# Performance work log

Hardware: AMD Instinct MI355X
Metric: run time of the kernel (lower is better)

## Reference

```python
import jax, jax.numpy as jnp
import numpy as np

B, S, D = 4, 2048, 1024
N_HEAD, D_HEAD = 16, 64


def setup_inputs() -> dict:
    key = jax.random.key(0)
    ks = jax.random.split(key, 9)
    sd = 0.02
    x = jax.random.normal(ks[0], (B, S, D), dtype=jnp.float32)
    # causal mask: True = masked (future positions)
    causal = jnp.triu(jnp.ones((S, S), dtype=bool), k=1)
    attn_mask = jnp.broadcast_to(causal, (B, S, S))
    Wq = jax.random.normal(ks[1], (D, N_HEAD * D_HEAD), dtype=jnp.float32) * sd
    bq = jnp.zeros((N_HEAD * D_HEAD,), dtype=jnp.float32)
    Wk = jax.random.normal(ks[2], (D, N_HEAD * D_HEAD), dtype=jnp.float32) * sd
    bk = jnp.zeros((N_HEAD * D_HEAD,), dtype=jnp.float32)
    Wv = jax.random.normal(ks[3], (D, N_HEAD * D_HEAD), dtype=jnp.float32) * sd
    bv = jnp.zeros((N_HEAD * D_HEAD,), dtype=jnp.float32)
    Wo = jax.random.normal(ks[4], (N_HEAD * D_HEAD, D), dtype=jnp.float32) * sd
    bo = jnp.zeros((D,), dtype=jnp.float32)
    return {"x": x, "attn_mask": attn_mask, "Wq": Wq, "bq": bq,
            "Wk": Wk, "bk": bk, "Wv": Wv, "bv": bv, "Wo": Wo, "bo": bo}


def reference(x, attn_mask, Wq, bq, Wk, bk, Wv, bv, Wo, bo):
    b, s, _ = x.shape
    scale = 1.0 / (D_HEAD ** 0.5)
    # QKV projections -> [b, n_head, s, d_head]
    def split_heads(y):
        return y.reshape(b, s, N_HEAD, D_HEAD).transpose(0, 2, 1, 3)
    q = split_heads(x @ Wq + bq)
    k = split_heads(x @ Wk + bk)
    v = split_heads(x @ Wv + bv)
    scores = jnp.einsum('bhqd,bhkd->bhqk', q, k) * scale
    scores = jnp.where(attn_mask[:, None, :, :], jnp.float32(-1e9), scores)
    attn_prob = jax.nn.softmax(scores, axis=-1)
    context = jnp.einsum('bhqk,bhkd->bhqd', attn_prob, v)
    context = context.transpose(0, 2, 1, 3).reshape(b, s, N_HEAD * D_HEAD)
    output = context @ Wo + bo
    return (output, attn_prob)
```

## Files before the change

kernel.cpp:

```cpp
#include <hip/hip_runtime.h>
#include <hip/hip_bf16.h>

typedef unsigned short u16;
typedef __attribute__((ext_vector_type(8))) short bf16x8;
typedef __attribute__((ext_vector_type(4))) float f32x4;

#define S_LEN  2048
#define DMODEL 1024
#define NHEAD  16
#define DH     64
#define BATCH  4
#define QBLK   128
#define KBLK   64
#define SWZ(row, c) (((c) ^ ((row) & 7)))

__device__ inline u16 f2bf(float f) {
  union { float f; unsigned u; } v; v.f = f;
  unsigned u = v.u;
  return (u16)((u + 0x7FFFu + ((u >> 16) & 1u)) >> 16);
}

__device__ inline f32x4 mfma16(bf16x8 a, bf16x8 b, f32x4 c) {
  return __builtin_amdgcn_mfma_f32_16x16x32_bf16(a, b, c, 0, 0, 0);
}

__device__ inline void gload_lds16(const u16* g, u16* l) {
  __builtin_amdgcn_global_load_lds(
      (const __attribute__((address_space(1))) void*)g,
      (__attribute__((address_space(3))) void*)l, 16, 0, 0);
}

__global__ __launch_bounds__(256) void k_convert_x(const float* __restrict__ x,
                                                   u16* __restrict__ xb) {
  int idx = blockIdx.x * 256 + threadIdx.x;
  const float4* p = (const float4*)(x + (size_t)idx * 8);
  float4 a = p[0], b = p[1];
  bf16x8 o;
  o[0] = (short)f2bf(a.x); o[1] = (short)f2bf(a.y);
  o[2] = (short)f2bf(a.z); o[3] = (short)f2bf(a.w);
  o[4] = (short)f2bf(b.x); o[5] = (short)f2bf(b.y);
  o[6] = (short)f2bf(b.z); o[7] = (short)f2bf(b.w);
  *(bf16x8*)(xb + (size_t)idx * 8) = o;
}

__global__ __launch_bounds__(256) void k_wT4(const float* __restrict__ W0,
                                             const float* __restrict__ W1,
                                             const float* __restrict__ W2,
                                             const float* __restrict__ W3,
                                             u16* __restrict__ WtBase) {
  __shared__ float T[32][33];
  int z = blockIdx.z;
  const float* W = (z == 0) ? W0 : (z == 1) ? W1 : (z == 2) ? W2 : W3;
  u16* Wt = WtBase + (size_t)z * DMODEL * DMODEL;
  int tx = threadIdx.x, ty = threadIdx.y;
  int n0 = blockIdx.x * 32, k0 = blockIdx.y * 32;
  for (int i = 0; i < 4; ++i)
    T[ty + i * 8][tx] = W[(size_t)(k0 + ty + i * 8) * DMODEL + n0 + tx];
  __syncthreads();
  for (int i = 0; i < 4; ++i)
    Wt[(size_t)(n0 + ty + i * 8) * DMODEL + k0 + tx] = f2bf(T[tx][ty + i * 8]);
}

__global__ __launch_bounds__(256) void k_gemm_qkv(const u16* __restrict__ A,
                                                  const u16* __restrict__ Wcat,
                                                  const float* __restrict__ bq,
                                                  const float* __restrict__ bk,
                                                  const float* __restrict__ bv,
                                                  u16* __restrict__ Qh,
                                                  u16* __restrict__ Kh,
                                                  u16* __restrict__ Vc) {
  const int K = 1024;
  __shared__ u16 As[128 * 32];
  __shared__ u16 Bs[128 * 32];
  int tid = threadIdx.x, w = tid >> 6, l = tid & 63;
  int f = blockIdx.x;
  int xcd = f & 7, i = f >> 3;
  int sb = i >> 6;
  int t = i & 63;
  int bm = xcd * 8 + (t & 7);
  int bn = sb * 8 + (t >> 3);
  int wr = w >> 1, wc = w & 1;
  f32x4 acc[4][4];
  for (int ii = 0; ii < 4; ++ii)
    for (int j = 0; j < 4; ++j) acc[ii][j] = (f32x4){0.f, 0.f, 0.f, 0.f};
  const u16* Ablk = A + (size_t)bm * 128 * K;
  const u16* Bblk = Wcat + (size_t)bn * 128 * K;

  for (int ks = 0; ks < K / 32; ++ks) {
    int k0 = ks * 32;
    __syncthreads();
    for (int r = 0; r < 2; ++r) {
      int c = r * 256 + tid;
      int row = c >> 2, c4 = c & 3;
      gload_lds16(Ablk + (size_t)row * K + k0 + c4 * 8, &As[c * 8]);
      gload_lds16(Bblk + (size_t)row * K + k0 + c4 * 8, &Bs[c * 8]);
    }
    __syncthreads();
    bf16x8 af[4], bfr[4];
    for (int mt = 0; mt < 4; ++mt)
      af[mt] = *(const bf16x8*)&As[(wr * 64 + mt * 16 + (l & 15)) * 32 + (l >> 4) * 8];
    for (int nt = 0; nt < 4; ++nt)
      bfr[nt] = *(const bf16x8*)&Bs[(wc * 64 + nt * 16 + (l & 15)) * 32 + (l >> 4) * 8];
    for (int mt = 0; mt < 4; ++mt)
      for (int nt = 0; nt < 4; ++nt)
        acc[mt][nt] = mfma16(af[mt], bfr[nt], acc[mt][nt]);
  }

  int region = (bn * 128) >> 10;
  const float* bias = (region == 0) ? bq : (region == 1) ? bk : bv;
  u16* dst = (region == 0) ? Qh : (region == 1) ? Kh : Vc;

  for (int mt = 0; mt < 4; ++mt)
    for (int nt = 0; nt < 4; ++nt) {
      int colg = bn * 128 + wc * 64 + nt * 16 + (l & 15);
      int col = colg & 1023;
      float bsv = bias[col];
      for (int r = 0; r < 4; ++r) {
        int row = bm * 128 + wr * 64 + mt * 16 + (l >> 4) * 4 + r;
        float v = acc[mt][nt][r] + bsv;
        if (region == 2) {
          dst[(size_t)row * 1024 + col] = f2bf(v);
        } else {
          int b = row >> 11, s = row & 2047, h = col >> 6, d = col & 63;
          dst[(((size_t)(b * NHEAD + h)) * S_LEN + s) * DH + d] = f2bf(v);
        }
      }
    }
}

__global__ __launch_bounds__(256) void k_gemm_out(const u16* __restrict__ A,
                                                  const u16* __restrict__ Bt,
                                                  const float* __restrict__ bias,
                                                  float* __restrict__ Cout) {
  const int K = 1024, N = 1024;
  __shared__ u16 As[128 * 32];
  __shared__ u16 Bs[128 * 32];
  int tid = threadIdx.x, w = tid >> 6, l = tid & 63;
  int f = blockIdx.x;
  int xcd = f & 7, i = f >> 3;
  int bm = xcd * 8 + (i & 7);
  int bn = i >> 3;
  int wr = w >> 1, wc = w & 1;
  f32x4 acc[4][4];
  for (int ii = 0; ii < 4; ++ii)
    for (int j = 0; j < 4; ++j) acc[ii][j] = (f32x4){0.f, 0.f, 0.f, 0.f};
  const u16* Ablk = A + (size_t)bm * 128 * K;
  const u16* Bblk = Bt + (size_t)bn * 128 * K;

  for (int ks = 0; ks < K / 32; ++ks) {
    int k0 = ks * 32;
    __syncthreads();
    for (int r = 0; r < 2; ++r) {
      int c = r * 256 + tid;
      int row = c >> 2, c4 = c & 3;
      gload_lds16(Ablk + (size_t)row * K + k0 + c4 * 8, &As[c * 8]);
      gload_lds16(Bblk + (size_t)row * K + k0 + c4 * 8, &Bs[c * 8]);
    }
    __syncthreads();
    bf16x8 af[4], bfr[4];
    for (int mt = 0; mt < 4; ++mt)
      af[mt] = *(const bf16x8*)&As[(wr * 64 + mt * 16 + (l & 15)) * 32 + (l >> 4) * 8];
    for (int nt = 0; nt < 4; ++nt)
      bfr[nt] = *(const bf16x8*)&Bs[(wc * 64 + nt * 16 + (l & 15)) * 32 + (l >> 4) * 8];
    for (int mt = 0; mt < 4; ++mt)
      for (int nt = 0; nt < 4; ++nt)
        acc[mt][nt] = mfma16(af[mt], bfr[nt], acc[mt][nt]);
  }

  for (int mt = 0; mt < 4; ++mt)
    for (int nt = 0; nt < 4; ++nt) {
      int col = bn * 128 + wc * 64 + nt * 16 + (l & 15);
      float bsv = bias[col];
      for (int r = 0; r < 4; ++r) {
        int row = bm * 128 + wr * 64 + mt * 16 + (l >> 4) * 4 + r;
        Cout[(size_t)row * N + col] = acc[mt][nt][r] + bsv;
      }
    }
}

__global__ __launch_bounds__(256) void k_vT(const u16* __restrict__ Vc,
                                            u16* __restrict__ Vt) {
  __shared__ u16 T[64][65];
  int bh = blockIdx.x, st = blockIdx.y;
  int b = bh >> 4, h = bh & 15;
  int s0 = st * 64;
  int tid = threadIdx.x;
  int row = tid >> 2, seg = tid & 3;
  const u16* src = Vc + ((size_t)(b * S_LEN + s0 + row)) * DMODEL + h * DH + seg * 16;
  bf16x8 v0 = *(const bf16x8*)src;
  bf16x8 v1 = *(const bf16x8*)(src + 8);
  for (int i = 0; i < 8; ++i) T[row][seg * 16 + i] = (u16)v0[i];
  for (int i = 0; i < 8; ++i) T[row][seg * 16 + 8 + i] = (u16)v1[i];
  __syncthreads();
  int d = row, sc = seg * 16;
  bf16x8 o0, o1;
  for (int i = 0; i < 8; ++i) o0[i] = (short)T[sc + i][d];
  for (int i = 0; i < 8; ++i) o1[i] = (short)T[sc + 8 + i][d];
  u16* dst = Vt + ((size_t)bh * DH + d) * S_LEN + s0 + sc;
  *(bf16x8*)dst = o0;
  *(bf16x8*)(dst + 8) = o1;
}


#define LOADK(KF, J0)                                                          \
  for (int kk_ = 0; kk_ < 2; ++kk_)                                            \
    for (int nt_ = 0; nt_ < 4; ++nt_)                                          \
      KF[kk_][nt_] = *(const bf16x8*)(Kg + (size_t)((J0) + nt_ * 16 + ln) * DH \
                                      + kk_ * 32 + lg * 8);

#define P1TILE(KF, J0)                                                         \
  {                                                                            \
    const int j0_ = (J0);                                                      \
    f32x4 acc[2][4];                                                           \
    for (int mt = 0; mt < 2; ++mt)                                             \
      for (int nt = 0; nt < 4; ++nt) acc[mt][nt] = (f32x4){0.f, 0.f, 0.f, 0.f};\
    for (int kk = 0; kk < 2; ++kk)                                             \
      for (int mt = 0; mt < 2; ++mt)                                           \
        for (int nt = 0; nt < 4; ++nt)                                         \
          acc[mt][nt] = mfma16(qf[mt][kk], KF[kk][nt], acc[mt][nt]);           \
    bool mask_ = (j0_ >= q0);                                                  \
    for (int mt = 0; mt < 2; ++mt)                                             \
      for (int r = 0; r < 4; ++r) {                                            \
        int rl = w * 32 + mt * 16 + lg * 4 + r;                                \
        float x0 = acc[mt][0][r] * scale2;                                     \
        float x1 = acc[mt][1][r] * scale2;                                     \
        float x2 = acc[mt][2][r] * scale2;                                     \
        float x3 = acc[mt][3][r] * scale2;                                     \
        if (mask_) {                                                           \
          if (j0_ + 0 + ln > q0 + rl) x0 = -1e9f;                              \
          if (j0_ + 16 + ln > q0 + rl) x1 = -1e9f;                             \
          if (j0_ + 32 + ln > q0 + rl) x2 = -1e9f;                             \
          if (j0_ + 48 + ln > q0 + rl) x3 = -1e9f;                             \
        }                                                                      \
        float s = __builtin_amdgcn_exp2f(x0) + __builtin_amdgcn_exp2f(x1) +    \
                  __builtin_amdgcn_exp2f(x2) + __builtin_amdgcn_exp2f(x3);     \
        s += __shfl_xor(s, 1);                                                 \
        s += __shfl_xor(s, 2);                                                 \
        s += __shfl_xor(s, 4);                                                 \
        s += __shfl_xor(s, 8);                                                 \
        lrow[mt][r] += s;                                                      \
      }                                                                        \
  }

#define P2TILE(KFC, KFN, KB, PRE)                                              \
  {                                                                            \
    const int j0_ = (KB) * KBLK;                                               \
    bf16x8 vb_[2][4];                                                          \
    for (int kk = 0; kk < 2; ++kk)                                             \
      for (int nt = 0; nt < 4; ++nt)                                           \
        vb_[kk][nt] = *(const bf16x8*)(Vg + (size_t)(nt * 16 + ln) * S_LEN +   \
                                       j0_ + kk * 32 + lg * 8);                \
    f32x4 acc[2][4];                                                           \
    for (int mt = 0; mt < 2; ++mt)                                             \
      for (int nt = 0; nt < 4; ++nt) acc[mt][nt] = (f32x4){0.f, 0.f, 0.f, 0.f};\
    for (int kk = 0; kk < 2; ++kk)                                             \
      for (int mt = 0; mt < 2; ++mt)                                           \
        for (int nt = 0; nt < 4; ++nt)                                         \
          acc[mt][nt] = mfma16(qf[mt][kk], KFC[kk][nt], acc[mt][nt]);          \
    if (PRE) { LOADK(KFN, j0_ + KBLK); }                                       \
    bool mask_ = (j0_ >= q0);                                                  \
    for (int mt = 0; mt < 2; ++mt)                                             \
      for (int r = 0; r < 4; ++r) {                                            \
        int rl = w * 32 + mt * 16 + lg * 4 + r;                                \
        float il = ilrow[mt][r];                                               \
        float* prow = Pg + (size_t)(q0 + rl) * S_LEN + j0_;                    \
        for (int nt = 0; nt < 4; ++nt) {                                       \
          int cl = nt * 16 + ln;                                               \
          float v = acc[mt][nt][r] * scale2;                                   \
          if (mask_ && (j0_ + cl > q0 + rl)) v = -1e9f;                        \
          float p = __builtin_amdgcn_exp2f(v) * il;                            \
          __builtin_nontemporal_store(p, prow + cl);                           \
          Ps[rl * 64 + SWZ(rl, cl >> 3) * 8 + (cl & 7)] = f2bf(p);             \
        }                                                                      \
      }                                                                        \
    for (int kk = 0; kk < 2; ++kk) {                                           \
      bf16x8 pa[2];                                                            \
      for (int mt = 0; mt < 2; ++mt) {                                         \
        int row = w * 32 + mt * 16 + ln;                                       \
        pa[mt] = *(const bf16x8*)&Ps[row * 64 + SWZ(row, kk * 4 + lg) * 8];    \
      }                                                                        \
      for (int mt = 0; mt < 2; ++mt)                                           \
        for (int nt = 0; nt < 4; ++nt)                                         \
          octx[mt][nt] = mfma16(pa[mt], vb_[kk][nt], octx[mt][nt]);            \
    }                                                                          \
  }

__global__ __launch_bounds__(256) void k_attn(const u16* __restrict__ Qh,
                                              const u16* __restrict__ Kh,
                                              const u16* __restrict__ Vt,
                                              float* __restrict__ P,
                                              u16* __restrict__ ctx) {
  __shared__ u16 Ps[QBLK * KBLK];

  int flat = blockIdx.x;
  int xcd = flat & 7, idx = flat >> 3;
  int bh = xcd * 8 + (idx >> 4);
  int qb = 15 - (idx & 15);
  int q0 = qb * QBLK;
  int tid = threadIdx.x, w = tid >> 6, l = tid & 63;
  const int lg = l >> 4, ln = l & 15;
  const u16* Qg = Qh + (size_t)bh * S_LEN * DH;
  const u16* Kg = Kh + (size_t)bh * S_LEN * DH;
  const u16* Vg = Vt + (size_t)bh * DH * S_LEN;
  float* Pg = P + (size_t)bh * S_LEN * S_LEN;

  bf16x8 qf[2][2];
  for (int mt = 0; mt < 2; ++mt)
    for (int kk = 0; kk < 2; ++kk)
      qf[mt][kk] = *(const bf16x8*)(Qg + (size_t)(q0 + w * 32 + mt * 16 + ln) * DH +
                                    kk * 32 + lg * 8);

  const int nkb = q0 / KBLK + QBLK / KBLK;
  const float scale2 = 0.18033688011112042f;

  float lrow[2][4];
  for (int mt = 0; mt < 2; ++mt)
    for (int r = 0; r < 4; ++r) lrow[mt][r] = 0.f;

  {
    bf16x8 kfA[2][4], kfB[2][4];
    LOADK(kfA, 0);
    for (int kb = 0; kb < nkb; kb += 2) {
      LOADK(kfB, (kb + 1) * KBLK);
      P1TILE(kfA, kb * KBLK);
      if (kb + 2 < nkb) LOADK(kfA, (kb + 2) * KBLK);
      P1TILE(kfB, (kb + 1) * KBLK);
    }
  }
  float ilrow[2][4];
  for (int mt = 0; mt < 2; ++mt)
    for (int r = 0; r < 4; ++r) ilrow[mt][r] = 1.f / lrow[mt][r];

  f32x4 octx[2][4];
  for (int mt = 0; mt < 2; ++mt)
    for (int nt = 0; nt < 4; ++nt) octx[mt][nt] = (f32x4){0.f, 0.f, 0.f, 0.f};

  {
    bf16x8 kfA[2][4], kfB[2][4];
    LOADK(kfA, 0);
    for (int kb = 0; kb < nkb; kb += 2) {
      P2TILE(kfA, kfB, kb, 1);
      P2TILE(kfB, kfA, kb + 1, (kb + 2) < nkb);
    }
  }

  int jz = nkb * KBLK;
  int ncol4 = (S_LEN - jz) >> 2;
  if (ncol4 > 0) {
    f32x4 z = (f32x4){0.f, 0.f, 0.f, 0.f};
    for (int rr = 0; rr < QBLK; ++rr) {
      float* prow = Pg + (size_t)(q0 + rr) * S_LEN + jz;
      for (int j4 = tid; j4 < ncol4; j4 += 256)
        __builtin_nontemporal_store(z, (f32x4*)(prow + j4 * 4));
    }
  }

  int b = bh >> 4, h = bh & 15;
  for (int mt = 0; mt < 2; ++mt)
    for (int nt = 0; nt < 4; ++nt)
      for (int r = 0; r < 4; ++r) {
        int rl = w * 32 + mt * 16 + lg * 4 + r;
        int d = nt * 16 + ln;
        ctx[((size_t)(b * S_LEN + q0 + rl)) * DMODEL + h * DH + d] =
            f2bf(octx[mt][nt][r]);
      }
}

extern "C" void kernel_launch(void* const* d_in, const int* in_sizes, int n_in,
                              void* d_out, int out_size, void* d_ws, size_t ws_size,
                              hipStream_t stream) {
  (void)in_sizes; (void)n_in; (void)out_size; (void)ws_size;
  const float* x  = (const float*)d_in[0];
  const float* Wq = (const float*)d_in[2];
  const float* bq = (const float*)d_in[3];
  const float* Wk = (const float*)d_in[4];
  const float* bk = (const float*)d_in[5];
  const float* Wv = (const float*)d_in[6];
  const float* bv = (const float*)d_in[7];
  const float* Wo = (const float*)d_in[8];
  const float* bo = (const float*)d_in[9];

  char* ws = (char*)d_ws;
  u16* xb   = (u16*)(ws);
  u16* Wcat = (u16*)(ws + 16777216);
  u16* WoT  = Wcat + 3 * (size_t)DMODEL * DMODEL;
  u16* Qh   = (u16*)(ws + 25165824);
  u16* Kh   = (u16*)(ws + 25165824 + 1 * 16777216);
  u16* Vc   = (u16*)(ws + 25165824 + 2 * 16777216);
  u16* Vt   = (u16*)(ws + 25165824 + 3 * 16777216);
  u16* ctx  = Vc;

  float* outp = (float*)d_out;
  float* Pg = outp + (size_t)BATCH * S_LEN * DMODEL;

  k_convert_x<<<4096, 256, 0, stream>>>(x, xb);
  dim3 wtb(32, 8), wtg(32, 32, 4);
  k_wT4<<<wtg, wtb, 0, stream>>>(Wq, Wk, Wv, Wo, Wcat);
  k_gemm_qkv<<<dim3(1536), 256, 0, stream>>>(xb, Wcat, bq, bk, bv, Qh, Kh, Vc);
  k_vT<<<dim3(64, 32), 256, 0, stream>>>(Vc, Vt);
  k_attn<<<dim3(1024), 256, 0, stream>>>(Qh, Kh, Vt, Pg, ctx);
  k_gemm_out<<<dim3(512), 256, 0, stream>>>(ctx, WoT, bo, outp);
}
```

Baseline: 457.8 us.

## Fuse V transpose into QKV GEMM epilogue and merge prep kernels

Merges the x-to-bf16 conversion and weight-transpose kernels into one launch. The QKV GEMM epilogue now writes V directly in transposed per-head layout through an LDS staging tile, which removes the separate V-transpose kernel and its extra global round trip. This drops two kernel launches and one intermediate buffer pass. In exchange the GEMM gains 16KB of LDS and extra barriers in the V blocks, and the LDS transpose reads use strided column access.

```diff
diff --git a/kernel.cpp b/kernel.cpp
--- a/kernel.cpp
+++ b/kernel.cpp
@@ -30,30 +30,33 @@
       (__attribute__((address_space(3))) void*)l, 16, 0, 0);
 }
 
-__global__ __launch_bounds__(256) void k_convert_x(const float* __restrict__ x,
-                                                   u16* __restrict__ xb) {
-  int idx = blockIdx.x * 256 + threadIdx.x;
-  const float4* p = (const float4*)(x + (size_t)idx * 8);
-  float4 a = p[0], b = p[1];
-  bf16x8 o;
-  o[0] = (short)f2bf(a.x); o[1] = (short)f2bf(a.y);
-  o[2] = (short)f2bf(a.z); o[3] = (short)f2bf(a.w);
-  o[4] = (short)f2bf(b.x); o[5] = (short)f2bf(b.y);
-  o[6] = (short)f2bf(b.z); o[7] = (short)f2bf(b.w);
-  *(bf16x8*)(xb + (size_t)idx * 8) = o;
-}
-
-__global__ __launch_bounds__(256) void k_wT4(const float* __restrict__ W0,
-                                             const float* __restrict__ W1,
-                                             const float* __restrict__ W2,
-                                             const float* __restrict__ W3,
-                                             u16* __restrict__ WtBase) {
+__global__ __launch_bounds__(256) void k_prep(const float* __restrict__ x,
+                                              u16* __restrict__ xb,
+                                              const float* __restrict__ W0,
+                                              const float* __restrict__ W1,
+                                              const float* __restrict__ W2,
+                                              const float* __restrict__ W3,
+                                              u16* __restrict__ WtBase) {
   __shared__ float T[32][33];
-  int z = blockIdx.z;
+  int blk = blockIdx.x, tid = threadIdx.x;
+  if (blk < 4096) {
+    int idx = blk * 256 + tid;
+    const float4* p = (const float4*)(x + (size_t)idx * 8);
+    float4 a = p[0], b = p[1];
+    bf16x8 o;
+    o[0] = (short)f2bf(a.x); o[1] = (short)f2bf(a.y);
+    o[2] = (short)f2bf(a.z); o[3] = (short)f2bf(a.w);
+    o[4] = (short)f2bf(b.x); o[5] = (short)f2bf(b.y);
+    o[6] = (short)f2bf(b.z); o[7] = (short)f2bf(b.w);
+    *(bf16x8*)(xb + (size_t)idx * 8) = o;
+    return;
+  }
+  int zi = blk - 4096;
+  int z = zi >> 10, rem = zi & 1023;
   const float* W = (z == 0) ? W0 : (z == 1) ? W1 : (z == 2) ? W2 : W3;
   u16* Wt = WtBase + (size_t)z * DMODEL * DMODEL;
-  int tx = threadIdx.x, ty = threadIdx.y;
-  int n0 = blockIdx.x * 32, k0 = blockIdx.y * 32;
+  int tx = tid & 31, ty = tid >> 5;
+  int n0 = (rem & 31) * 32, k0 = (rem >> 5) * 32;
   for (int i = 0; i < 4; ++i)
     T[ty + i * 8][tx] = W[(size_t)(k0 + ty + i * 8) * DMODEL + n0 + tx];
   __syncthreads();
@@ -68,10 +71,11 @@
                                                   const float* __restrict__ bv,
                                                   u16* __restrict__ Qh,
                                                   u16* __restrict__ Kh,
-                                                  u16* __restrict__ Vc) {
+                                                  u16* __restrict__ Vt) {
   const int K = 1024;
   __shared__ u16 As[128 * 32];
   __shared__ u16 Bs[128 * 32];
+  __shared__ u16 Ts[128 * 64];
   int tid = threadIdx.x, w = tid >> 6, l = tid & 63;
   int f = blockIdx.x;
   int xcd = f & 7, i = f >> 3;
@@ -107,25 +111,53 @@
   }
 
   int region = (bn * 128) >> 10;
-  const float* bias = (region == 0) ? bq : (region == 1) ? bk : bv;
-  u16* dst = (region == 0) ? Qh : (region == 1) ? Kh : Vc;
-
-  for (int mt = 0; mt < 4; ++mt)
-    for (int nt = 0; nt < 4; ++nt) {
-      int colg = bn * 128 + wc * 64 + nt * 16 + (l & 15);
-      int col = colg & 1023;
-      float bsv = bias[col];
-      for (int r = 0; r < 4; ++r) {
-        int row = bm * 128 + wr * 64 + mt * 16 + (l >> 4) * 4 + r;
-        float v = acc[mt][nt][r] + bsv;
-        if (region == 2) {
-          dst[(size_t)row * 1024 + col] = f2bf(v);
-        } else {
+
+  if (region != 2) {
+    const float* bias = (region == 0) ? bq : bk;
+    u16* dst = (region == 0) ? Qh : Kh;
+    for (int mt = 0; mt < 4; ++mt)
+      for (int nt = 0; nt < 4; ++nt) {
+        int colg = bn * 128 + wc * 64 + nt * 16 + (l & 15);
+        int col = colg & 1023;
+        float bsv = bias[col];
+        for (int r = 0; r < 4; ++r) {
+          int row = bm * 128 + wr * 64 + mt * 16 + (l >> 4) * 4 + r;
+          float v = acc[mt][nt][r] + bsv;
           int b = row >> 11, s = row & 2047, h = col >> 6, d = col & 63;
           dst[(((size_t)(b * NHEAD + h)) * S_LEN + s) * DH + d] = f2bf(v);
         }
       }
-    }
+  } else {
+    int hbase = (bn - 16) * 2;
+    int b = bm >> 4, s0 = (bm & 15) * 128;
+    for (int half = 0; half < 2; ++half) {
+      __syncthreads();
+      if (wc == half) {
+        for (int mt = 0; mt < 4; ++mt)
+          for (int nt = 0; nt < 4; ++nt) {
+            int cl = nt * 16 + (l & 15);
+            float bsv = bv[(hbase + half) * 64 + cl];
+            for (int r = 0; r < 4; ++r) {
+              int rl = wr * 64 + mt * 16 + (l >> 4) * 4 + r;
+              Ts[rl * 64 + cl] = f2bf(acc[mt][nt][r] + bsv);
+            }
+          }
+      }
+      __syncthreads();
+      int d = tid >> 2, seg = tid & 3;
+      int h = hbase + half;
+      u16* dst = Vt + (((size_t)(b * NHEAD + h)) * DH + d) * S_LEN + s0 + seg * 32;
+      bf16x8 o0, o1, o2, o3;
+      for (int k = 0; k < 8; ++k) o0[k] = (short)Ts[(seg * 32 + k) * 64 + d];
+      for (int k = 0; k < 8; ++k) o1[k] = (short)Ts[(seg * 32 + 8 + k) * 64 + d];
+      for (int k = 0; k < 8; ++k) o2[k] = (short)Ts[(seg * 32 + 16 + k) * 64 + d];
+      for (int k = 0; k < 8; ++k) o3[k] = (short)Ts[(seg * 32 + 24 + k) * 64 + d];
+      *(bf16x8*)dst = o0;
+      *(bf16x8*)(dst + 8) = o1;
+      *(bf16x8*)(dst + 16) = o2;
+      *(bf16x8*)(dst + 24) = o3;
+    }
+  }
 }
 
 __global__ __launch_bounds__(256) void k_gemm_out(const u16* __restrict__ A,
@@ -176,29 +208,6 @@
         Cout[(size_t)row * N + col] = acc[mt][nt][r] + bsv;
       }
     }
-}
-
-__global__ __launch_bounds__(256) void k_vT(const u16* __restrict__ Vc,
-                                            u16* __restrict__ Vt) {
-  __shared__ u16 T[64][65];
-  int bh = blockIdx.x, st = blockIdx.y;
-  int b = bh >> 4, h = bh & 15;
-  int s0 = st * 64;
-  int tid = threadIdx.x;
-  int row = tid >> 2, seg = tid & 3;
-  const u16* src = Vc + ((size_t)(b * S_LEN + s0 + row)) * DMODEL + h * DH + seg * 16;
-  bf16x8 v0 = *(const bf16x8*)src;
-  bf16x8 v1 = *(const bf16x8*)(src + 8);
-  for (int i = 0; i < 8; ++i) T[row][seg * 16 + i] = (u16)v0[i];
-  for (int i = 0; i < 8; ++i) T[row][seg * 16 + 8 + i] = (u16)v1[i];
-  __syncthreads();
-  int d = row, sc = seg * 16;
-  bf16x8 o0, o1;
-  for (int i = 0; i < 8; ++i) o0[i] = (short)T[sc + i][d];
-  for (int i = 0; i < 8; ++i) o1[i] = (short)T[sc + 8 + i][d];
-  u16* dst = Vt + ((size_t)bh * DH + d) * S_LEN + s0 + sc;
-  *(bf16x8*)dst = o0;
-  *(bf16x8*)(dst + 8) = o1;
 }
 
 
@@ -386,18 +395,14 @@
   u16* WoT  = Wcat + 3 * (size_t)DMODEL * DMODEL;
   u16* Qh   = (u16*)(ws + 25165824);
   u16* Kh   = (u16*)(ws + 25165824 + 1 * 16777216);
-  u16* Vc   = (u16*)(ws + 25165824 + 2 * 16777216);
+  u16* ctx  = (u16*)(ws + 25165824 + 2 * 16777216);
   u16* Vt   = (u16*)(ws + 25165824 + 3 * 16777216);
-  u16* ctx  = Vc;
 
   float* outp = (float*)d_out;
   float* Pg = outp + (size_t)BATCH * S_LEN * DMODEL;
 
-  k_convert_x<<<4096, 256, 0, stream>>>(x, xb);
-  dim3 wtb(32, 8), wtg(32, 32, 4);
-  k_wT4<<<wtg, wtb, 0, stream>>>(Wq, Wk, Wv, Wo, Wcat);
-  k_gemm_qkv<<<dim3(1536), 256, 0, stream>>>(xb, Wcat, bq, bk, bv, Qh, Kh, Vc);
-  k_vT<<<dim3(64, 32), 256, 0, stream>>>(Vc, Vt);
+  k_prep<<<dim3(8192), 256, 0, stream>>>(x, xb, Wq, Wk, Wv, Wo, Wcat);
+  k_gemm_qkv<<<dim3(1536), 256, 0, stream>>>(xb, Wcat, bq, bk, bv, Qh, Kh, Vt);
   k_attn<<<dim3(1024), 256, 0, stream>>>(Qh, Kh, Vt, Pg, ctx);
   k_gemm_out<<<dim3(512), 256, 0, stream>>>(ctx, WoT, bo, outp);
 }
```

Result: no change. 461.9 us (+0.9%).
